# Performance work log

Hardware: AMD Instinct MI355X
Metric: run time of the kernel (lower is better)

## Reference

```python
import math
import jax, jax.numpy as jnp
import numpy as np

B, S, D, H = 2, 2048, 1024, 16
DK = D // H  # 64


def _rope_tables(seq_len, d_k):
    inv_freq = 1.0 / (10000.0 ** (jnp.arange(0, d_k, 2, dtype=jnp.float32) / d_k))
    t = jnp.arange(seq_len, dtype=jnp.float32)
    freqs = t[:, None] * inv_freq[None, :]          # [S, d_k/2]
    emb = jnp.concatenate([freqs, freqs], axis=-1)  # [S, d_k]
    return jnp.cos(emb), jnp.sin(emb)


def _rotate_half(x):
    x1, x2 = jnp.split(x, 2, axis=-1)
    return jnp.concatenate([-x2, x1], axis=-1)


def setup_inputs() -> dict:
    key = jax.random.key(0)
    ks = jax.random.split(key, 11)
    sc = 1.0 / math.sqrt(D)
    inp = {
        'query': jax.random.normal(ks[0], (B, S, D), jnp.float32),
        'key': jax.random.normal(ks[1], (B, S, D), jnp.float32),
        'value': jax.random.normal(ks[2], (B, S, D), jnp.float32),
        'mask': jnp.tril(jnp.ones((S, S), bool))[None, None, :, :],  # causal [1,1,S,S]
        'Wq': jax.random.normal(ks[3], (D, D), jnp.float32) * sc,
        'bq': jnp.zeros((D,), jnp.float32),
        'Wk': jax.random.normal(ks[4], (D, D), jnp.float32) * sc,
        'bk': jnp.zeros((D,), jnp.float32),
        'Wv': jax.random.normal(ks[5], (D, D), jnp.float32) * sc,
        'bv': jnp.zeros((D,), jnp.float32),
        'Wo': jax.random.normal(ks[6], (D, D), jnp.float32) * sc,
        'bo': jnp.zeros((D,), jnp.float32),
    }
    return inp


def reference(query, key, value, mask, Wq, bq, Wk, bk, Wv, bv, Wo, bo):
    b, s, d = query.shape
    # QKV projections -> [b, H, s, DK]
    def proj(x, W, bias):
        y = x @ W.T + bias
        return y.reshape(b, s, H, DK).transpose(0, 2, 1, 3)
    q = proj(query, Wq, bq)
    k = proj(key, Wk, bk)
    v = proj(value, Wv, bv)
    # inline RoPE
    cos, sin = _rope_tables(s, DK)          # [s, DK]
    cos = cos[None, None]; sin = sin[None, None]
    q = q * cos + _rotate_half(q) * sin
    k = k * cos + _rotate_half(k) * sin
    # naive O(N^2) attention (dropout disabled: eval-mode reference)
    scores = jnp.einsum('bhqd,bhkd->bhqk', q, k) / math.sqrt(DK)
    scores = jnp.where(mask, scores, jnp.float32(-1e9))
    p = jax.nn.softmax(scores, axis=-1)
    x = jnp.einsum('bhqk,bhkd->bhqd', p, v)
    x = x.transpose(0, 2, 1, 3).reshape(b, s, d)
    return x @ Wo.T + bo
```

## Files before the change

kernel.cpp:

```cpp
#include <hip/hip_runtime.h>
#include <hip/hip_bf16.h>
#include <math.h>

typedef unsigned short u16;
typedef unsigned int u32;
typedef __attribute__((ext_vector_type(4))) float f32x4;
typedef __attribute__((ext_vector_type(4))) short bf16x4;
typedef __attribute__((ext_vector_type(8))) short bf16x8;
typedef __attribute__((ext_vector_type(8))) unsigned short u16x8;

constexpr int Bc = 2, Sc = 2048, Dc = 1024, Hc = 16, DKc = 64, Mc = 4096;

__device__ __forceinline__ u16 f2bf(float f) {
  __hip_bfloat16 h = __float2bfloat16(f);
  return __builtin_bit_cast(u16, h);
}

__device__ __forceinline__ void gll16(const u16* g, const u16* l) {
  __builtin_amdgcn_global_load_lds((const __attribute__((address_space(1))) void*)g,
                                   (__attribute__((address_space(3))) void*)l, 16, 0, 0);
}

__device__ __forceinline__ bf16x8 frag_swz(const u16* tile, int row, int col) {
  const int sw = (row & 7) << 3;
  const int base = row * 64 + col;
  bf16x4 lo = *(const bf16x4*)(tile + (base ^ sw));
  bf16x4 hi = *(const bf16x4*)(tile + ((base + 16) ^ sw));
  return __builtin_shufflevector(lo, hi, 0, 1, 2, 3, 4, 5, 6, 7);
}

__global__ __launch_bounds__(256) void cast_many(
    const float* __restrict__ i0, const float* __restrict__ i1,
    const float* __restrict__ i2, const float* __restrict__ i3,
    u16* __restrict__ o0, u16* __restrict__ o1,
    u16* __restrict__ o2, u16* __restrict__ o3, int n8)
{
  const int z = blockIdx.y;
  const float* in = z == 0 ? i0 : z == 1 ? i1 : z == 2 ? i2 : i3;
  u16* out = z == 0 ? o0 : z == 1 ? o1 : z == 2 ? o2 : o3;
  const int i = blockIdx.x * 256 + threadIdx.x;
  if (i >= n8) return;
  const float4* p = (const float4*)in + (size_t)i * 2;
  const float4 a = p[0], b = p[1];
  u16x8 o;
  o[0] = f2bf(a.x); o[1] = f2bf(a.y); o[2] = f2bf(a.z); o[3] = f2bf(a.w);
  o[4] = f2bf(b.x); o[5] = f2bf(b.y); o[6] = f2bf(b.z); o[7] = f2bf(b.w);
  ((u16x8*)out)[i] = o;
}

__device__ __forceinline__ void gemm_remap(int& row0, int& col0) {
  const int flat = blockIdx.x + gridDim.x * blockIdx.y;
  const int loc = flat >> 3;
  row0 = ((flat & 7) * 4 + (loc & 3)) * 128;
  col0 = (loc >> 2) * 128;
}

__device__ __forceinline__ void gemm_core(
    const u16* __restrict__ X, const u16* __restrict__ W,
    u16* smem, int row0, int col0, f32x4 (&acc)[2][4])
{
  const int tid = threadIdx.x;
  const int w = tid >> 6, lane = tid & 63;
  const int l15 = lane & 15, l4 = lane >> 4;
  const int wr = w >> 1, wc = w & 1;

  auto stage = [&](int buf, int k0) {
    u16* dA = smem + buf * 8192;
    u16* dB = smem + 16384 + buf * 8192;
#pragma unroll
    for (int s = 0; s < 2; ++s) {
      const int c = s * 512 + w * 64 + lane;
      const int r = c >> 3;
      const int cc = (c & 7) ^ (r & 7);
      gll16(X + (size_t)(row0 + r) * Dc + k0 + cc * 8, dA + (s * 512 + w * 64) * 8);
      gll16(W + (size_t)(col0 + r) * Dc + k0 + cc * 8, dB + (s * 512 + w * 64) * 8);
    }
  };

  stage(0, 0);
  __syncthreads();

  for (int kt = 0; kt < Dc / 64; ++kt) {
    const int cur = kt & 1;
    if (kt + 1 < Dc / 64) stage(cur ^ 1, (kt + 1) * 64);
    const u16* At = smem + cur * 8192;
    const u16* Bt = smem + 16384 + cur * 8192;
#pragma unroll
    for (int ks = 0; ks < 2; ++ks) {
      bf16x8 af[2], bfr[4];
#pragma unroll
      for (int m = 0; m < 2; ++m)
        af[m] = frag_swz(At, wr * 32 + m * 16 + l15, ks * 32 + l4 * 4);
#pragma unroll
      for (int n = 0; n < 4; ++n)
        bfr[n] = frag_swz(Bt, wc * 64 + n * 16 + l15, ks * 32 + l4 * 4);
#pragma unroll
      for (int m = 0; m < 2; ++m)
#pragma unroll
        for (int n = 0; n < 4; ++n)
          acc[m][n] = __builtin_amdgcn_mfma_f32_16x16x32_bf16(af[m], bfr[n], acc[m][n], 0, 0, 0);
    }
    __syncthreads();
  }
}

__global__ __launch_bounds__(512) void gemm_qkv(
    const u16* __restrict__ xq, const u16* __restrict__ xk, const u16* __restrict__ xv,
    const u16* __restrict__ wq, const u16* __restrict__ wk, const u16* __restrict__ wv,
    const float* __restrict__ bq, const float* __restrict__ bk, const float* __restrict__ bv,
    u16* __restrict__ Qb, u16* __restrict__ Kb, u16* __restrict__ Vt)
{
  __shared__ u16 smem[4 * 128 * 64];
  const int z = blockIdx.z;
  const u16* X = z == 0 ? xq : z == 1 ? xk : xv;
  const u16* W = z == 0 ? wq : z == 1 ? wk : wv;
  const float* bias = z == 0 ? bq : z == 1 ? bk : bv;

  const int tid = threadIdx.x;
  const int w = tid >> 6, lane = tid & 63;
  const int l15 = lane & 15, l4 = lane >> 4;
  const int wr = w >> 1, wc = w & 1;
  int row0, col0;
  gemm_remap(row0, col0);

  f32x4 acc[2][4] = {};
  gemm_core(X, W, smem, row0, col0, acc);

  if (z < 2) {
    u16* Out = z == 0 ? Qb : Kb;
    const int h = (col0 >> 6) + wc;
#pragma unroll
    for (int m = 0; m < 2; ++m)
#pragma unroll
      for (int i = 0; i < 4; ++i) {
        const int row = row0 + wr * 32 + m * 16 + 4 * l4 + i;
        const int srow = row & (Sc - 1);
        const size_t obase = ((size_t)((row >> 11) * Hc + h) * Sc + srow) * DKc;
        float vv[4];
#pragma unroll
        for (int n = 0; n < 4; ++n)
          vv[n] = acc[m][n][i] + bias[col0 + wc * 64 + n * 16 + l15];
        float cs[2], sn[2];
#pragma unroll
        for (int hf = 0; hf < 2; ++hf) {
          const int jj = hf * 16 + l15;
          const float ang = (float)srow * exp2f((float)jj * (-13.287712379549449f / 32.0f));
          sincosf(ang, &sn[hf], &cs[hf]);
        }
#pragma unroll
        for (int n = 0; n < 4; ++n) {
          const float rot = (n < 2) ? -vv[n ^ 2] : vv[n ^ 2];
          const float o = vv[n] * cs[n & 1] + rot * sn[n & 1];
          Out[obase + n * 16 + l15] = f2bf(o);
        }
      }
  } else {
    u16* T = smem;
    __syncthreads();
#pragma unroll
    for (int m = 0; m < 2; ++m)
#pragma unroll
      for (int i = 0; i < 4; ++i) {
        const int r = wr * 32 + m * 16 + 4 * l4 + i;
#pragma unroll
        for (int n = 0; n < 4; ++n) {
          const int c = wc * 64 + n * 16 + l15;
          T[c * 132 + r] = f2bf(acc[m][n][i] + bias[col0 + c]);
        }
      }
    __syncthreads();
    const int bidx = row0 >> 11, srow0 = row0 & (Sc - 1);
    const int c = tid >> 2, rq = (tid & 3) * 32;
    const int h = (col0 >> 6) + (c >> 6);
    const int dk = c & 63;
    u16* gdst = Vt + ((size_t)(bidx * Hc + h) * DKc + dk) * Sc + srow0 + rq;
#pragma unroll
    for (int u = 0; u < 4; ++u)
      *(u16x8*)(gdst + u * 8) = *(const u16x8*)&T[c * 132 + rq + u * 8];
  }
}

__global__ __launch_bounds__(512) void gemm_out(
    const u16* __restrict__ X, const u16* __restrict__ W,
    const float* __restrict__ bias, float* __restrict__ Out)
{
  __shared__ u16 smem[4 * 128 * 64];
  const int tid = threadIdx.x;
  const int w = tid >> 6, lane = tid & 63;
  const int l15 = lane & 15, l4 = lane >> 4;
  const int wr = w >> 1, wc = w & 1;
  int row0, col0;
  gemm_remap(row0, col0);

  f32x4 acc[2][4] = {};
  gemm_core(X, W, smem, row0, col0, acc);

#pragma unroll
  for (int m = 0; m < 2; ++m)
#pragma unroll
    for (int i = 0; i < 4; ++i) {
      const int row = row0 + wr * 32 + m * 16 + 4 * l4 + i;
#pragma unroll
      for (int n = 0; n < 4; ++n) {
        const int col = col0 + wc * 64 + n * 16 + l15;
        Out[(size_t)row * Dc + col] = acc[m][n][i] + bias[col];
      }
    }
}

__global__ __launch_bounds__(256) void attn_mfma(
    const u16* __restrict__ Qb, const u16* __restrict__ Kb,
    const u16* __restrict__ Vt, u16* __restrict__ Xb)
{
  __shared__ u16 smem[24576];
  u16* Qs = smem + 16384;

  const int tid = threadIdx.x;
  const int w = tid >> 6, lane = tid & 63;
  const int l15 = lane & 15, l4 = lane >> 4;

  const int d = blockIdx.x + gridDim.x * blockIdx.y;
  const int loc = d >> 3;
  const int bh = (d & 7) * 4 + (loc & 3);
  const int qt = 31 - (loc >> 2);
  const int q0 = qt * 64;
  const u16* Qg = Qb + ((size_t)bh * Sc + q0) * DKc;
  const u16* Kg = Kb + (size_t)bh * Sc * DKc;
  const u16* Vg = Vt + (size_t)bh * DKc * Sc;
  const int nk = qt + 1;

#pragma unroll
  for (int s = 0; s < 2; ++s) {
    const int c = s * 256 + tid;
    const int r = c >> 3, cc = (c & 7) ^ (r & 7);
    gll16(Qg + (size_t)r * DKc + cc * 8, Qs + c * 8);
  }
  auto stageKV = [&](int buf, int k0) {
    u16* Kd = smem + (buf == 0 ? 0 : buf == 1 ? 8192 : 16384);
    u16* Vd = smem + (buf == 0 ? 4096 : buf == 1 ? 12288 : 20480);
#pragma unroll
    for (int s = 0; s < 2; ++s) {
      const int c = s * 256 + tid;
      const int r = c >> 3, cc = (c & 7) ^ (r & 7);
      gll16(Kg + (size_t)(k0 + r) * DKc + cc * 8, Kd + c * 8);
      gll16(Vg + (size_t)r * Sc + k0 + cc * 8,   Vd + c * 8);
    }
  };
  stageKV(0, 0);
  __syncthreads();

  bf16x8 aq[2];
#pragma unroll
  for (int ks = 0; ks < 2; ++ks)
    aq[ks] = frag_swz(Qs, w * 16 + l15, ks * 32 + l4 * 4);

  if (nk > 1) stageKV(1, 64);

  auto QK = [&](f32x4 (&dst)[4], int buf) {
    const u16* Kt = smem + (buf == 0 ? 0 : buf == 1 ? 8192 : 16384);
#pragma unroll
    for (int ks = 0; ks < 2; ++ks) {
      bf16x8 bk[4];
#pragma unroll
      for (int n = 0; n < 4; ++n)
        bk[n] = frag_swz(Kt, n * 16 + l15, ks * 32 + l4 * 4);
#pragma unroll
      for (int n = 0; n < 4; ++n)
        dst[n] = __builtin_amdgcn_mfma_f32_16x16x32_bf16(bk[n], aq[ks], dst[n], 0, 0, 0);
    }
  };

  f32x4 sA[4] = {}, sB[4] = {};
  QK(sA, 0);

  f32x4 aco[4] = {};
  float mreg = -INFINITY, lreg = 0.f;
  constexpr float C2 = 0.18033688011112042f;

  auto ITER = [&](int t, f32x4 (&cur)[4], f32x4 (&nxt)[4]) {
    __syncthreads();
    const int tb = t - (t / 3) * 3;
    if (t + 2 < nk) stageKV(tb + 2 >= 3 ? tb - 1 : tb + 2, (t + 2) * 64);
    if (t + 1 < nk) {
#pragma unroll
      for (int n = 0; n < 4; ++n) nxt[n] = f32x4{0.f, 0.f, 0.f, 0.f};
      QK(nxt, tb + 1 >= 3 ? tb - 2 : tb + 1);
    }

    const bool mtile = (t == nk - 1);
    const int k0t = t * 64;
    const int q = q0 + w * 16 + l15;
    float rm = -INFINITY;
#pragma unroll
    for (int n = 0; n < 4; ++n)
#pragma unroll
      for (int i = 0; i < 4; ++i) {
        float s = cur[n][i] * C2;
        if (mtile && (k0t + n * 16 + 4 * l4 + i) > q) s = -1e30f;
        cur[n][i] = s;
        rm = fmaxf(rm, s);
      }
    rm = fmaxf(rm, __shfl_xor(rm, 16, 64));
    rm = fmaxf(rm, __shfl_xor(rm, 32, 64));

    const bool need = __any(rm > mreg + 8.0f);
    float corr = 1.f;
    if (need) {
      const float mnew = fmaxf(mreg, rm);
      corr = exp2f(mreg - mnew);
      mreg = mnew;
    }
    float rs = 0.f;
#pragma unroll
    for (int n = 0; n < 4; ++n)
#pragma unroll
      for (int i = 0; i < 4; ++i) {
        const float p = exp2f(cur[n][i] - mreg);
        cur[n][i] = p;
        rs += p;
      }
    rs += __shfl_xor(rs, 16, 64);
    rs += __shfl_xor(rs, 32, 64);
    lreg = lreg * corr + rs;
    if (need) {
#pragma unroll
      for (int i = 0; i < 4; ++i) {
        const float c = __shfl(corr, 4 * l4 + i, 64);
#pragma unroll
        for (int n = 0; n < 4; ++n) aco[n][i] *= c;
      }
    }

    bf16x8 pa[2];
#pragma unroll
    for (int ks = 0; ks < 2; ++ks) {
      bf16x8 tt;
#pragma unroll
      for (int j = 0; j < 8; ++j)
        tt[j] = (short)f2bf(cur[ks * 2 + (j >> 2)][j & 3]);
      pa[ks] = tt;
    }

    const u16* Vc = smem + (tb == 0 ? 4096 : tb == 1 ? 12288 : 20480);
#pragma unroll
    for (int ks = 0; ks < 2; ++ks) {
      bf16x8 bv[4];
#pragma unroll
      for (int n = 0; n < 4; ++n)
        bv[n] = frag_swz(Vc, n * 16 + l15, ks * 32 + l4 * 4);
#pragma unroll
      for (int n = 0; n < 4; ++n)
        aco[n] = __builtin_amdgcn_mfma_f32_16x16x32_bf16(pa[ks], bv[n], aco[n], 0, 0, 0);
    }
  };

  int t = 0;
  while (true) {
    ITER(t, sA, sB);
    if (++t >= nk) break;
    ITER(t, sB, sA);
    if (++t >= nk) break;
  }

  const int bidx = bh >> 4, h = bh & 15;
  const float invl = 1.0f / lreg;
#pragma unroll
  for (int i = 0; i < 4; ++i) {
    const int q = q0 + w * 16 + 4 * l4 + i;
    const float inv = __shfl(invl, 4 * l4 + i, 64);
#pragma unroll
    for (int n = 0; n < 4; ++n)
      Xb[((size_t)bidx * Sc + q) * Dc + h * DKc + n * 16 + l15] = f2bf(aco[n][i] * inv);
  }
}

extern "C" void kernel_launch(void* const* d_in, const int* in_sizes, int n_in,
                              void* d_out, int out_size, void* d_ws, size_t ws_size,
                              hipStream_t stream) {
  const float* query = (const float*)d_in[0];
  const float* key   = (const float*)d_in[1];
  const float* value = (const float*)d_in[2];
  const float* Wq = (const float*)d_in[4];
  const float* bq = (const float*)d_in[5];
  const float* Wk = (const float*)d_in[6];
  const float* bk = (const float*)d_in[7];
  const float* Wv = (const float*)d_in[8];
  const float* bv = (const float*)d_in[9];
  const float* Wo = (const float*)d_in[10];
  const float* bo = (const float*)d_in[11];

  const size_t MD = (size_t)Mc * Dc;
  const size_t DD = (size_t)Dc * Dc;
  u16* xq = (u16*)d_ws;
  u16* xk = xq + MD;
  u16* xv = xk + MD;
  u16* wq = xv + MD;
  u16* wk = wq + DD;
  u16* wv = wk + DD;
  u16* wo = wv + DD;
  u16* Qb = wo + DD;
  u16* Kb = Qb + MD;
  u16* Vt = Kb + MD;
  u16* Xb = Vt + MD;

  cast_many<<<dim3(MD / 2048, 3), 256, 0, stream>>>(
      query, key, value, nullptr, xq, xk, xv, nullptr, (int)(MD / 8));
  cast_many<<<dim3(DD / 2048, 4), 256, 0, stream>>>(
      Wq, Wk, Wv, Wo, wq, wk, wv, wo, (int)(DD / 8));

  gemm_qkv<<<dim3(32, 8, 3), 512, 0, stream>>>(
      xq, xk, xv, wq, wk, wv, bq, bk, bv, Qb, Kb, Vt);
  attn_mfma<<<dim3(32, 32), 256, 0, stream>>>(Qb, Kb, Vt, Xb);
  gemm_out<<<dim3(32, 8), 512, 0, stream>>>(Xb, wo, bo, (float*)d_out);
}
```

Baseline: 232.3 us.

## Single-buffer QKV GEMM smem for occupancy and fold softmax scale into Q

Templates the GEMM core so the QKV projection uses a single-buffered shared-memory tile (smaller LDS footprint, sized to fit the V transpose staging), trading prefetch overlap for more resident blocks per CU. Separately, the softmax scale (1/sqrt(dk)·log2 e) is multiplied into Q during the RoPE epilogue, which removes a per-score multiply in the attention loop. The single-buffer path adds a barrier per k-step and exposes load latency. Pre-scaling Q before bf16 rounding slightly changes numerics.

Measured after the change: 238.3 us. 2.6% more time.

```diff
diff --git a/kernel.cpp b/kernel.cpp
--- a/kernel.cpp
+++ b/kernel.cpp
@@ -55,6 +55,7 @@
   col0 = (loc >> 2) * 128;
 }
 
+template <bool SB>
 __device__ __forceinline__ void gemm_core(
     const u16* __restrict__ X, const u16* __restrict__ W,
     u16* smem, int row0, int col0, f32x4 (&acc)[2][4])
@@ -65,8 +66,8 @@
   const int wr = w >> 1, wc = w & 1;
 
   auto stage = [&](int buf, int k0) {
-    u16* dA = smem + buf * 8192;
-    u16* dB = smem + 16384 + buf * 8192;
+    u16* dA = smem + (SB ? 0 : buf * 8192);
+    u16* dB = smem + (SB ? 8192 : 16384 + buf * 8192);
 #pragma unroll
     for (int s = 0; s < 2; ++s) {
       const int c = s * 512 + w * 64 + lane;
@@ -76,15 +77,9 @@
       gll16(W + (size_t)(col0 + r) * Dc + k0 + cc * 8, dB + (s * 512 + w * 64) * 8);
     }
   };
-
-  stage(0, 0);
-  __syncthreads();
-
-  for (int kt = 0; kt < Dc / 64; ++kt) {
-    const int cur = kt & 1;
-    if (kt + 1 < Dc / 64) stage(cur ^ 1, (kt + 1) * 64);
-    const u16* At = smem + cur * 8192;
-    const u16* Bt = smem + 16384 + cur * 8192;
+  auto compute = [&](int buf) {
+    const u16* At = smem + (SB ? 0 : buf * 8192);
+    const u16* Bt = smem + (SB ? 8192 : 16384 + buf * 8192);
 #pragma unroll
     for (int ks = 0; ks < 2; ++ks) {
       bf16x8 af[2], bfr[4];
@@ -100,7 +95,24 @@
         for (int n = 0; n < 4; ++n)
           acc[m][n] = __builtin_amdgcn_mfma_f32_16x16x32_bf16(af[m], bfr[n], acc[m][n], 0, 0, 0);
     }
+  };
+
+  if constexpr (SB) {
+    for (int kt = 0; kt < Dc / 64; ++kt) {
+      stage(0, kt * 64);
+      __syncthreads();
+      compute(0);
+      __syncthreads();
+    }
+  } else {
+    stage(0, 0);
     __syncthreads();
+    for (int kt = 0; kt < Dc / 64; ++kt) {
+      const int cur = kt & 1;
+      if (kt + 1 < Dc / 64) stage(cur ^ 1, (kt + 1) * 64);
+      compute(cur);
+      __syncthreads();
+    }
   }
 }
 
@@ -110,7 +122,7 @@
     const float* __restrict__ bq, const float* __restrict__ bk, const float* __restrict__ bv,
     u16* __restrict__ Qb, u16* __restrict__ Kb, u16* __restrict__ Vt)
 {
-  __shared__ u16 smem[4 * 128 * 64];
+  __shared__ u16 smem[17408];
   const int z = blockIdx.z;
   const u16* X = z == 0 ? xq : z == 1 ? xk : xv;
   const u16* W = z == 0 ? wq : z == 1 ? wk : wv;
@@ -124,10 +136,11 @@
   gemm_remap(row0, col0);
 
   f32x4 acc[2][4] = {};
-  gemm_core(X, W, smem, row0, col0, acc);
+  gemm_core<true>(X, W, smem, row0, col0, acc);
 
   if (z < 2) {
     u16* Out = z == 0 ? Qb : Kb;
+    const float qs = (z == 0) ? 0.18033688011112042f : 1.f;
     const int h = (col0 >> 6) + wc;
 #pragma unroll
     for (int m = 0; m < 2; ++m)
@@ -150,7 +163,7 @@
 #pragma unroll
         for (int n = 0; n < 4; ++n) {
           const float rot = (n < 2) ? -vv[n ^ 2] : vv[n ^ 2];
-          const float o = vv[n] * cs[n & 1] + rot * sn[n & 1];
+          const float o = (vv[n] * cs[n & 1] + rot * sn[n & 1]) * qs;
           Out[obase + n * 16 + l15] = f2bf(o);
         }
       }
@@ -184,7 +197,7 @@
     const u16* __restrict__ X, const u16* __restrict__ W,
     const float* __restrict__ bias, float* __restrict__ Out)
 {
-  __shared__ u16 smem[4 * 128 * 64];
+  __shared__ u16 smem[32768];
   const int tid = threadIdx.x;
   const int w = tid >> 6, lane = tid & 63;
   const int l15 = lane & 15, l4 = lane >> 4;
@@ -193,7 +206,7 @@
   gemm_remap(row0, col0);
 
   f32x4 acc[2][4] = {};
-  gemm_core(X, W, smem, row0, col0, acc);
+  gemm_core<false>(X, W, smem, row0, col0, acc);
 
 #pragma unroll
   for (int m = 0; m < 2; ++m)
@@ -275,7 +288,6 @@
 
   f32x4 aco[4] = {};
   float mreg = -INFINITY, lreg = 0.f;
-  constexpr float C2 = 0.18033688011112042f;
 
   auto ITER = [&](int t, f32x4 (&cur)[4], f32x4 (&nxt)[4]) {
     __syncthreads();
@@ -295,7 +307,7 @@
     for (int n = 0; n < 4; ++n)
 #pragma unroll
       for (int i = 0; i < 4; ++i) {
-        float s = cur[n][i] * C2;
+        float s = cur[n][i];
         if (mtile && (k0t + n * 16 + 4 * l4 + i) > q) s = -1e30f;
         cur[n][i] = s;
         rm = fmaxf(rm, s);
```

## Fold softmax scale into Q projection and compute row sums via MFMA

Applied to the files above, without the earlier changes.

Moves the 1/sqrt(dk)*log2e scaling into the Q projection epilogue so the attention loop no longer multiplies every score. The per-row sum of probabilities is now accumulated by an extra MFMA against a ones vector instead of VALU adds and cross-lane shuffles, and the max reduction uses three-input max trees. This trims VALU work in the softmax critical path at the cost of one extra MFMA per k-step and rounding of scaled Q to bf16.

New measurement: 237.2 us. 1.02x slower.

```diff
diff --git a/kernel.cpp b/kernel.cpp
--- a/kernel.cpp
+++ b/kernel.cpp
@@ -14,6 +14,10 @@
 __device__ __forceinline__ u16 f2bf(float f) {
   __hip_bfloat16 h = __float2bfloat16(f);
   return __builtin_bit_cast(u16, h);
+}
+
+__device__ __forceinline__ float max3f(float a, float b, float c) {
+  return fmaxf(fmaxf(a, b), c);
 }
 
 __device__ __forceinline__ void gll16(const u16* g, const u16* l) {
@@ -128,6 +132,7 @@
 
   if (z < 2) {
     u16* Out = z == 0 ? Qb : Kb;
+    const float qs = (z == 0) ? 0.18033688011112042f : 1.f;
     const int h = (col0 >> 6) + wc;
 #pragma unroll
     for (int m = 0; m < 2; ++m)
@@ -150,7 +155,7 @@
 #pragma unroll
         for (int n = 0; n < 4; ++n) {
           const float rot = (n < 2) ? -vv[n ^ 2] : vv[n ^ 2];
-          const float o = vv[n] * cs[n & 1] + rot * sn[n & 1];
+          const float o = (vv[n] * cs[n & 1] + rot * sn[n & 1]) * qs;
           Out[obase + n * 16 + l15] = f2bf(o);
         }
       }
@@ -274,8 +279,9 @@
   QK(sA, 0);
 
   f32x4 aco[4] = {};
-  float mreg = -INFINITY, lreg = 0.f;
-  constexpr float C2 = 0.18033688011112042f;
+  f32x4 c5 = {};
+  float mreg = -INFINITY;
+  const bf16x8 vones = (short)0x3F80;
 
   auto ITER = [&](int t, f32x4 (&cur)[4], f32x4 (&nxt)[4]) {
     __syncthreads();
@@ -287,49 +293,42 @@
       QK(nxt, tb + 1 >= 3 ? tb - 2 : tb + 1);
     }
 
-    const bool mtile = (t == nk - 1);
-    const int k0t = t * 64;
-    const int q = q0 + w * 16 + l15;
-    float rm = -INFINITY;
-#pragma unroll
-    for (int n = 0; n < 4; ++n)
-#pragma unroll
-      for (int i = 0; i < 4; ++i) {
-        float s = cur[n][i] * C2;
-        if (mtile && (k0t + n * 16 + 4 * l4 + i) > q) s = -1e30f;
-        cur[n][i] = s;
-        rm = fmaxf(rm, s);
-      }
+    if (t == nk - 1) {
+      const int k0t = t * 64;
+      const int q = q0 + w * 16 + l15;
+#pragma unroll
+      for (int n = 0; n < 4; ++n)
+#pragma unroll
+        for (int i = 0; i < 4; ++i)
+          if ((k0t + n * 16 + 4 * l4 + i) > q) cur[n][i] = -1e30f;
+    }
+    const float a0 = max3f(cur[0][0], cur[0][1], cur[0][2]);
+    const float a1 = max3f(cur[0][3], cur[1][0], cur[1][1]);
+    const float a2 = max3f(cur[1][2], cur[1][3], cur[2][0]);
+    const float a3 = max3f(cur[2][1], cur[2][2], cur[2][3]);
+    const float a4 = max3f(cur[3][0], cur[3][1], cur[3][2]);
+    float rm = max3f(max3f(a0, a1, a2), fmaxf(a3, a4), cur[3][3]);
     rm = fmaxf(rm, __shfl_xor(rm, 16, 64));
     rm = fmaxf(rm, __shfl_xor(rm, 32, 64));
 
     const bool need = __any(rm > mreg + 8.0f);
-    float corr = 1.f;
     if (need) {
       const float mnew = fmaxf(mreg, rm);
-      corr = exp2f(mreg - mnew);
+      const float corr = exp2f(mreg - mnew);
       mreg = mnew;
-    }
-    float rs = 0.f;
-#pragma unroll
-    for (int n = 0; n < 4; ++n)
-#pragma unroll
-      for (int i = 0; i < 4; ++i) {
-        const float p = exp2f(cur[n][i] - mreg);
-        cur[n][i] = p;
-        rs += p;
-      }
-    rs += __shfl_xor(rs, 16, 64);
-    rs += __shfl_xor(rs, 32, 64);
-    lreg = lreg * corr + rs;
-    if (need) {
 #pragma unroll
       for (int i = 0; i < 4; ++i) {
         const float c = __shfl(corr, 4 * l4 + i, 64);
 #pragma unroll
         for (int n = 0; n < 4; ++n) aco[n][i] *= c;
+        c5[i] *= c;
       }
     }
+#pragma unroll
+    for (int n = 0; n < 4; ++n)
+#pragma unroll
+      for (int i = 0; i < 4; ++i)
+        cur[n][i] = exp2f(cur[n][i] - mreg);
 
     bf16x8 pa[2];
 #pragma unroll
@@ -351,6 +350,7 @@
 #pragma unroll
       for (int n = 0; n < 4; ++n)
         aco[n] = __builtin_amdgcn_mfma_f32_16x16x32_bf16(pa[ks], bv[n], aco[n], 0, 0, 0);
+      c5 = __builtin_amdgcn_mfma_f32_16x16x32_bf16(pa[ks], vones, c5, 0, 0, 0);
     }
   };
 
@@ -363,11 +363,10 @@
   }
 
   const int bidx = bh >> 4, h = bh & 15;
-  const float invl = 1.0f / lreg;
 #pragma unroll
   for (int i = 0; i < 4; ++i) {
     const int q = q0 + w * 16 + 4 * l4 + i;
-    const float inv = __shfl(invl, 4 * l4 + i, 64);
+    const float inv = 1.0f / c5[i];
 #pragma unroll
     for (int n = 0; n < 4; ++n)
       Xb[((size_t)bidx * Sc + q) * Dc + h * DKc + n * 16 + l15] = f2bf(aco[n][i] * inv);
```
